# Optimization experiments

Measured on AMD Instinct MI355X. Metric: run time of the kernel, lower is better.

## Reference

```python
import jax, jax.numpy as jnp
import numpy as np

IN_FEATURES = 8192
OUT_FEATURES = 8192
CODESZ = 8
CB_SIZE = 256


def fwht(x):
    """Orthonormal Walsh-Hadamard transform along last dim (power of 2).
    Equivalent to x @ H / sqrt(n) with Sylvester Hadamard H (symmetric),
    so it implements both matmul_hadU and matmul_hadUt for K=1."""
    b, n = x.shape
    h = 2
    while h <= n:
        x = x.reshape(b, n // h, h)
        half = h // 2
        a, c = x[..., :half], x[..., half:]
        x = jnp.concatenate([a + c, a - c], axis=-1)
        h *= 2
    return x.reshape(b, n) * jnp.asarray(1.0 / np.sqrt(n), x.dtype)


def setup_inputs() -> dict:
    key = jax.random.key(0)
    ks = jax.random.split(key, 8)
    inp = jax.random.normal(ks[0], (32, 4, IN_FEATURES), dtype=jnp.float16)
    Qidxs = jax.random.randint(ks[1], (OUT_FEATURES, IN_FEATURES // CODESZ), 0, CB_SIZE, dtype=jnp.int32)
    codebook_table = jax.random.normal(ks[2], (CB_SIZE, CODESZ), dtype=jnp.float32).astype(jnp.float16)
    # positive per-column rescale (scaleWH buffer)
    scaleWH = (0.5 + jax.random.uniform(ks[3], (IN_FEATURES,), dtype=jnp.float32)).astype(jnp.float16)
    # random sign vectors SU/SV (stored as int8 +-1 in torch; used as fp16 multipliers)
    SU = jnp.where(jax.random.uniform(ks[4], (IN_FEATURES,)) < 0.5, -1.0, 1.0).astype(jnp.float16)
    SV = jnp.where(jax.random.uniform(ks[5], (OUT_FEATURES,)) < 0.5, -1.0, 1.0).astype(jnp.float16)
    Wscale = jnp.asarray(0.02, dtype=jnp.float16)
    bias = (0.01 * jax.random.normal(ks[6], (OUT_FEATURES,), dtype=jnp.float32)).astype(jnp.float16)
    return {"input": inp, "Qidxs": Qidxs, "codebook_table": codebook_table,
            "scaleWH": scaleWH, "SU": SU, "SV": SV, "Wscale": Wscale, "bias": bias}


def reference(input, Qidxs, codebook_table, scaleWH, SU, SV, Wscale, bias):
    x = input.reshape(-1, IN_FEATURES).astype(jnp.float16)
    # rescale_WH + SU sign flip, fused elementwise
    x = (x / scaleWH) * SU
    # matmul_hadUt_cuda (in_features is a power of 2 -> pure orthonormal WHT)
    x = fwht(x)
    # codebook dequant + GEMM: W_hat[o, i] = codebook[Qidxs[o, i//8], i%8] * Wscale
    W_hat = codebook_table[Qidxs].reshape(OUT_FEATURES, IN_FEATURES) * Wscale  # [out, in] fp16
    out = x @ W_hat.T  # [tokens, out]
    # matmul_hadU_cuda on output side (power of 2, no truncation needed)
    out = fwht(out)
    out = out * SV + bias
    return out.reshape(input.shape[:-1] + (OUT_FEATURES,))
```

## Files before the change

kernel.cpp:

```cpp
#include <hip/hip_runtime.h>
#include <hip/hip_bf16.h>

#define IN_F 8192
#define OUT_F 8192
#define NROWS 128
#define CB 256
#define NSL 8
#define KSLICE (IN_F / NSL)
#define NTB 128
#define QC (IN_F / 8)

using bf8   = __attribute__((ext_vector_type(8))) short;
using f32x4 = __attribute__((ext_vector_type(4))) float;

typedef const __attribute__((address_space(1))) void* as1cv;
typedef __attribute__((address_space(3))) void* as3v;

__device__ inline float bf2f(unsigned int u) {
    union { unsigned int i; float f; } v; v.i = u << 16; return v.f;
}
__device__ inline unsigned short f2bf(float f) {
    __hip_bfloat16 h = __float2bfloat16(f);
    return *reinterpret_cast<unsigned short*>(&h);
}
__device__ inline void unpack8(uint4 v, float* f) {
    f[0] = bf2f(v.x & 0xffffu); f[1] = bf2f(v.x >> 16);
    f[2] = bf2f(v.y & 0xffffu); f[3] = bf2f(v.y >> 16);
    f[4] = bf2f(v.z & 0xffffu); f[5] = bf2f(v.z >> 16);
    f[6] = bf2f(v.w & 0xffffu); f[7] = bf2f(v.w >> 16);
}

#define FWHT_SCALE 0.011048543456039806f

#define FWHT16(v)                                                         \
    _Pragma("unroll")                                                     \
    for (int hb = 0; hb < 4; ++hb) {                                      \
        const int hh = 1 << hb;                                           \
        _Pragma("unroll")                                                 \
        for (int j = 0; j < 16; ++j)                                      \
            if (!(j & hh)) {                                              \
                float a_ = v[j], b_ = v[j | hh];                          \
                v[j] = a_ + b_; v[j | hh] = a_ - b_;                      \
            }                                                             \
    }

__device__ inline void fwht4096(float* v, float* lds, int t) {
    FWHT16(v)
#pragma unroll
    for (int e = 0; e < 16; ++e) lds[e * 260 + t] = v[e];
    __syncthreads();
    {
        const int base = (t & 15) * 260 + (t >> 4) * 16;
#pragma unroll
        for (int q = 0; q < 4; ++q) {
            float4 f = *reinterpret_cast<const float4*>(&lds[base + q * 4]);
            v[q * 4 + 0] = f.x; v[q * 4 + 1] = f.y;
            v[q * 4 + 2] = f.z; v[q * 4 + 3] = f.w;
        }
    }
    FWHT16(v)
    __syncthreads();
    {
        const int e = t & 15, ub = t >> 4;
#pragma unroll
        for (int i = 0; i < 16; ++i) lds[e * 260 + i * 16 + ub] = v[i];
    }
    __syncthreads();
    {
        const int e = t & 15, i = t >> 4;
#pragma unroll
        for (int ub = 0; ub < 16; ++ub) v[ub] = lds[e * 260 + i * 16 + ub];
    }
    FWHT16(v)
    __syncthreads();
    {
        const int e = t & 15, i = t >> 4;
#pragma unroll
        for (int ub = 0; ub < 16; ++ub) lds[ub * 260 + i * 16 + e] = v[ub];
    }
    __syncthreads();
    {
        const int base = (t >> 4) * 260 + (t & 15) * 16;
#pragma unroll
        for (int q = 0; q < 4; ++q) {
            float4 f = *reinterpret_cast<const float4*>(&lds[base + q * 4]);
            v[q * 4 + 0] = f.x; v[q * 4 + 1] = f.y;
            v[q * 4 + 2] = f.z; v[q * 4 + 3] = f.w;
        }
    }
}

__global__ __launch_bounds__(256) void k_pre4(const float* __restrict__ in,
                                              const float* __restrict__ scaleWH,
                                              const float* __restrict__ SU,
                                              unsigned short* __restrict__ xt) {
    __shared__ float lds[4160];
    const int r = blockIdx.x, h = blockIdx.y, t = threadIdx.x;
    float v[16];
    const float4* xp = reinterpret_cast<const float4*>(in + (size_t)r * IN_F);
    const float4* sp = reinterpret_cast<const float4*>(scaleWH);
    const float4* up = reinterpret_cast<const float4*>(SU);
#pragma unroll
    for (int q = 0; q < 4; ++q) {
        float4 xl = xp[t * 4 + q],        sl = sp[t * 4 + q],        ul = up[t * 4 + q];
        float4 xh = xp[1024 + t * 4 + q], sh = sp[1024 + t * 4 + q], uh = up[1024 + t * 4 + q];
        float lo0 = xl.x / sl.x * ul.x, hi0 = xh.x / sh.x * uh.x;
        float lo1 = xl.y / sl.y * ul.y, hi1 = xh.y / sh.y * uh.y;
        float lo2 = xl.z / sl.z * ul.z, hi2 = xh.z / sh.z * uh.z;
        float lo3 = xl.w / sl.w * ul.w, hi3 = xh.w / sh.w * uh.w;
        v[q * 4 + 0] = h ? lo0 - hi0 : lo0 + hi0;
        v[q * 4 + 1] = h ? lo1 - hi1 : lo1 + hi1;
        v[q * 4 + 2] = h ? lo2 - hi2 : lo2 + hi2;
        v[q * 4 + 3] = h ? lo3 - hi3 : lo3 + hi3;
    }
    fwht4096(v, lds, t);
    const int ub = t >> 4, i = t & 15;
    const int kblk = h * 128 + ub * 8 + (i >> 1);
    const size_t base = ((size_t)(r >> 4) * 256 + kblk) * 512 + (size_t)(r & 15) * 8;
#pragma unroll
    for (int half = 0; half < 2; ++half) {
        unsigned int w[4];
#pragma unroll
        for (int p = 0; p < 4; ++p) {
            unsigned int lo = f2bf(v[half * 8 + 2 * p]     * FWHT_SCALE);
            unsigned int hi = f2bf(v[half * 8 + 2 * p + 1] * FWHT_SCALE);
            w[p] = lo | (hi << 16);
        }
        const int oct = (i & 1) * 2 + half;
        *reinterpret_cast<uint4*>(xt + base + oct * 128) = make_uint4(w[0], w[1], w[2], w[3]);
    }
}

__global__ __launch_bounds__(512, 4) void k_gemm9(
        const unsigned short* __restrict__ xt,
        const int* __restrict__ Qidxs,
        const float* __restrict__ cb,
        const float* __restrict__ wscale,
        unsigned short* __restrict__ pout) {
    __shared__ __align__(16) unsigned short cbl[CB][8];
    __shared__ __align__(16) int Qlds[2][128 * 64];
    const int tid = threadIdx.x;
    const int wave = tid >> 6, lane = tid & 63;
    const int wr = wave & 3, wc = wave >> 2;
    const int lr = lane & 15, lk8 = lane >> 4;
    const int n0 = blockIdx.x * NTB;
    const int ks0 = blockIdx.y * KSLICE;
    const int ksb = ks0 >> 5;
    const int c0 = ks0 >> 3;

    auto stageQ = [&](int buf, int ch) {
#pragma unroll
        for (int j = 0; j < 4; ++j) {
            const int row = j * 32 + wave * 4 + (lane >> 4);
            const int cgs = (lane & 15) ^ (row & 15);
            const int* g = Qidxs + (size_t)(n0 + row) * QC + c0 + ch * 64 + cgs * 4;
            as3v l = (as3v)(&Qlds[buf][(j * 32 + wave * 4) * 64]);
            __builtin_amdgcn_global_load_lds((as1cv)(const void*)g, l, 16, 0, 0);
        }
    };

    stageQ(0, 0);
    const float wsc = wscale[0];
    for (int e = tid; e < CB * 8; e += 512) cbl[e >> 3][e & 7] = f2bf(cb[e] * wsc);

    f32x4 acc[2][4];
#pragma unroll
    for (int mt = 0; mt < 2; ++mt)
#pragma unroll
        for (int nt = 0; nt < 4; ++nt) acc[mt][nt] = (f32x4){0.f, 0.f, 0.f, 0.f};

    const unsigned short* xw = xt + ((size_t)(wr * 2) * 256 + ksb) * 512 + lane * 8;
    __syncthreads();
    stageQ(1, 1);

#define CHUNK(BUF, CH)                                                        \
    _Pragma("unroll")                                                         \
    for (int itc = 0; itc < 16; ++itc) {                                      \
        const int it = (CH) * 16 + itc;                                       \
        const int qcol = ((itc ^ lr) << 2) + lk8;                             \
        const int qv0 = Qlds[BUF][(wc * 64 +  0 + lr) * 64 + qcol];           \
        const int qv1 = Qlds[BUF][(wc * 64 + 16 + lr) * 64 + qcol];           \
        const int qv2 = Qlds[BUF][(wc * 64 + 32 + lr) * 64 + qcol];           \
        const int qv3 = Qlds[BUF][(wc * 64 + 48 + lr) * 64 + qcol];           \
        bf8 a0 = *reinterpret_cast<const bf8*>(xw + ((size_t)(0 * 256) + it) * 512); \
        bf8 a1 = *reinterpret_cast<const bf8*>(xw + ((size_t)(1 * 256) + it) * 512); \
        bf8 b0 = *(const bf8*)&cbl[qv0][0];                                   \
        bf8 b1 = *(const bf8*)&cbl[qv1][0];                                   \
        bf8 b2 = *(const bf8*)&cbl[qv2][0];                                   \
        bf8 b3 = *(const bf8*)&cbl[qv3][0];                                   \
        acc[0][0] = __builtin_amdgcn_mfma_f32_16x16x32_bf16(a0, b0, acc[0][0], 0, 0, 0); \
        acc[0][1] = __builtin_amdgcn_mfma_f32_16x16x32_bf16(a0, b1, acc[0][1], 0, 0, 0); \
        acc[0][2] = __builtin_amdgcn_mfma_f32_16x16x32_bf16(a0, b2, acc[0][2], 0, 0, 0); \
        acc[0][3] = __builtin_amdgcn_mfma_f32_16x16x32_bf16(a0, b3, acc[0][3], 0, 0, 0); \
        acc[1][0] = __builtin_amdgcn_mfma_f32_16x16x32_bf16(a1, b0, acc[1][0], 0, 0, 0); \
        acc[1][1] = __builtin_amdgcn_mfma_f32_16x16x32_bf16(a1, b1, acc[1][1], 0, 0, 0); \
        acc[1][2] = __builtin_amdgcn_mfma_f32_16x16x32_bf16(a1, b2, acc[1][2], 0, 0, 0); \
        acc[1][3] = __builtin_amdgcn_mfma_f32_16x16x32_bf16(a1, b3, acc[1][3], 0, 0, 0); \
    }

    CHUNK(0, 0)
    __syncthreads();
    CHUNK(1, 1)
#undef CHUNK

    unsigned short* ps = pout + (size_t)blockIdx.y * (NROWS * OUT_F);
#pragma unroll
    for (int mt = 0; mt < 2; ++mt) {
        const int row = wr * 32 + mt * 16 + lk8 * 4;
#pragma unroll
        for (int nt = 0; nt < 4; ++nt) {
            const int col = n0 + wc * 64 + nt * 16 + lr;
#pragma unroll
            for (int r2 = 0; r2 < 4; ++r2)
                ps[(size_t)(row + r2) * OUT_F + col] = f2bf(acc[mt][nt][r2]);
        }
    }
}

__global__ __launch_bounds__(256) void k_post4(const unsigned short* __restrict__ pin,
                                               const float* __restrict__ SV,
                                               const float* __restrict__ bias,
                                               float* __restrict__ out) {
    __shared__ float lds[4160];
    const int r = blockIdx.x, h = blockIdx.y, t = threadIdx.x;
    float lo[16], hi[16], v[16];
#pragma unroll
    for (int j = 0; j < 16; ++j) { lo[j] = 0.f; hi[j] = 0.f; }
#pragma unroll 1
    for (int sl = 0; sl < NSL; ++sl) {
        const uint4* pl = reinterpret_cast<const uint4*>(
            pin + (size_t)sl * NROWS * OUT_F + (size_t)r * OUT_F + t * 16);
        const uint4* ph = reinterpret_cast<const uint4*>(
            pin + (size_t)sl * NROWS * OUT_F + (size_t)r * OUT_F + 4096 + t * 16);
        float a[8], b[8];
        unpack8(pl[0], a); unpack8(pl[1], b);
#pragma unroll
        for (int j = 0; j < 8; ++j) { lo[j] += a[j]; lo[8 + j] += b[j]; }
        unpack8(ph[0], a); unpack8(ph[1], b);
#pragma unroll
        for (int j = 0; j < 8; ++j) { hi[j] += a[j]; hi[8 + j] += b[j]; }
    }
#pragma unroll
    for (int j = 0; j < 16; ++j) v[j] = h ? lo[j] - hi[j] : lo[j] + hi[j];
    fwht4096(v, lds, t);
    const int cb4 = (h * 4096 + (t >> 4) * 256 + (t & 15) * 16) >> 2;
    const float4* svp = reinterpret_cast<const float4*>(SV);
    const float4* bip = reinterpret_cast<const float4*>(bias);
    float4* op = reinterpret_cast<float4*>(out + (size_t)r * OUT_F);
#pragma unroll
    for (int q = 0; q < 4; ++q) {
        float4 sv = svp[cb4 + q], bi = bip[cb4 + q], o;
        o.x = v[q * 4 + 0] * FWHT_SCALE * sv.x + bi.x;
        o.y = v[q * 4 + 1] * FWHT_SCALE * sv.y + bi.y;
        o.z = v[q * 4 + 2] * FWHT_SCALE * sv.z + bi.z;
        o.w = v[q * 4 + 3] * FWHT_SCALE * sv.w + bi.w;
        op[cb4 + q] = o;
    }
}

extern "C" void kernel_launch(void* const* d_in, const int* in_sizes, int n_in,
                              void* d_out, int out_size, void* d_ws, size_t ws_size,
                              hipStream_t stream) {
    const float* in      = (const float*)d_in[0];
    const int*   Qidxs   = (const int*)d_in[1];
    const float* cb      = (const float*)d_in[2];
    const float* scaleWH = (const float*)d_in[3];
    const float* SU      = (const float*)d_in[4];
    const float* SV      = (const float*)d_in[5];
    const float* wscale  = (const float*)d_in[6];
    const float* bias    = (const float*)d_in[7];
    float* out = (float*)d_out;

    unsigned short* xt    = (unsigned short*)d_ws;
    unsigned short* parts = (unsigned short*)((char*)d_ws
                            + (size_t)NROWS * IN_F * 2);

    k_pre4<<<dim3(NROWS, 2), 256, 0, stream>>>(in, scaleWH, SU, xt);
    k_gemm9<<<dim3(OUT_F / NTB, NSL), 512, 0, stream>>>(xt, Qidxs, cb, wscale, parts);
    k_post4<<<dim3(NROWS, 2), 256, 0, stream>>>(parts, SV, bias, out);
}
```

Baseline: 46.33 us.

## Switch codebook GEMM to 32x32x16 MFMA with 4 waves and software pipelining

Moves the GEMM from 16x16x32 MFMA tiles with 8 waves to 32x32x16 MFMA tiles with 4 waves, each wave owning 32 output columns and all 128 rows. The preprocessing kernel writes the activation layout to match the new A-operand fragment order. The inner loop is restructured to double-buffer codebook lookups and activation loads across even and odd k-steps. The aim is fewer LDS codebook gathers per FLOP and better latency hiding, at the cost of more accumulator registers and lower occupancy per block.

```diff
diff --git a/kernel.cpp b/kernel.cpp
--- a/kernel.cpp
+++ b/kernel.cpp
@@ -10,8 +10,8 @@
 #define NTB 128
 #define QC (IN_F / 8)
 
-using bf8   = __attribute__((ext_vector_type(8))) short;
-using f32x4 = __attribute__((ext_vector_type(4))) float;
+using bf8    = __attribute__((ext_vector_type(8))) short;
+using f32x16 = __attribute__((ext_vector_type(16))) float;
 
 typedef const __attribute__((address_space(1))) void* as1cv;
 typedef __attribute__((address_space(3))) void* as3v;
@@ -90,7 +90,7 @@
     }
 }
 
-__global__ __launch_bounds__(256) void k_pre4(const float* __restrict__ in,
+__global__ __launch_bounds__(256) void k_pre5(const float* __restrict__ in,
                                               const float* __restrict__ scaleWH,
                                               const float* __restrict__ SU,
                                               unsigned short* __restrict__ xt) {
@@ -114,9 +114,8 @@
         v[q * 4 + 3] = h ? lo3 - hi3 : lo3 + hi3;
     }
     fwht4096(v, lds, t);
-    const int ub = t >> 4, i = t & 15;
-    const int kblk = h * 128 + ub * 8 + (i >> 1);
-    const size_t base = ((size_t)(r >> 4) * 256 + kblk) * 512 + (size_t)(r & 15) * 8;
+    const int k0 = h * 4096 + (t >> 4) * 256 + (t & 15) * 16;
+    const size_t base = ((size_t)(r >> 5) * 512 + (k0 >> 4)) * 512 + (size_t)(r & 31) * 8;
 #pragma unroll
     for (int half = 0; half < 2; ++half) {
         unsigned int w[4];
@@ -126,95 +125,107 @@
             unsigned int hi = f2bf(v[half * 8 + 2 * p + 1] * FWHT_SCALE);
             w[p] = lo | (hi << 16);
         }
-        const int oct = (i & 1) * 2 + half;
-        *reinterpret_cast<uint4*>(xt + base + oct * 128) = make_uint4(w[0], w[1], w[2], w[3]);
-    }
-}
-
-__global__ __launch_bounds__(512, 4) void k_gemm9(
+        *reinterpret_cast<uint4*>(xt + base + half * 256) = make_uint4(w[0], w[1], w[2], w[3]);
+    }
+}
+
+__global__ __launch_bounds__(256, 2) void k_gemm12(
         const unsigned short* __restrict__ xt,
         const int* __restrict__ Qidxs,
         const float* __restrict__ cb,
         const float* __restrict__ wscale,
         unsigned short* __restrict__ pout) {
     __shared__ __align__(16) unsigned short cbl[CB][8];
-    __shared__ __align__(16) int Qlds[2][128 * 64];
+    __shared__ __align__(16) int Qlds[2][8192];
     const int tid = threadIdx.x;
     const int wave = tid >> 6, lane = tid & 63;
-    const int wr = wave & 3, wc = wave >> 2;
-    const int lr = lane & 15, lk8 = lane >> 4;
+    const int ln31 = lane & 31, lh = lane >> 5;
     const int n0 = blockIdx.x * NTB;
     const int ks0 = blockIdx.y * KSLICE;
-    const int ksb = ks0 >> 5;
+    const int ksb2 = ks0 >> 4;
     const int c0 = ks0 >> 3;
 
-    auto stageQ = [&](int buf, int ch) {
-#pragma unroll
-        for (int j = 0; j < 4; ++j) {
-            const int row = j * 32 + wave * 4 + (lane >> 4);
-            const int cgs = (lane & 15) ^ (row & 15);
-            const int* g = Qidxs + (size_t)(n0 + row) * QC + c0 + ch * 64 + cgs * 4;
-            as3v l = (as3v)(&Qlds[buf][(j * 32 + wave * 4) * 64]);
+    auto stageQ = [&](int h) {
+#pragma unroll
+        for (int j = 0; j < 8; ++j) {
+            const int row = j * 16 + wave * 4 + (lane >> 4);
+            const int cgs = (lane & 15) ^ (row & 7);
+            const int* g = Qidxs + (size_t)(n0 + row) * QC + c0 + h * 64 + cgs * 4;
+            as3v l = (as3v)(&Qlds[h][(j * 16 + wave * 4) * 64]);
             __builtin_amdgcn_global_load_lds((as1cv)(const void*)g, l, 16, 0, 0);
         }
     };
 
-    stageQ(0, 0);
+    stageQ(0);
     const float wsc = wscale[0];
-    for (int e = tid; e < CB * 8; e += 512) cbl[e >> 3][e & 7] = f2bf(cb[e] * wsc);
-
-    f32x4 acc[2][4];
-#pragma unroll
-    for (int mt = 0; mt < 2; ++mt)
-#pragma unroll
-        for (int nt = 0; nt < 4; ++nt) acc[mt][nt] = (f32x4){0.f, 0.f, 0.f, 0.f};
-
-    const unsigned short* xw = xt + ((size_t)(wr * 2) * 256 + ksb) * 512 + lane * 8;
-    __syncthreads();
-    stageQ(1, 1);
-
-#define CHUNK(BUF, CH)                                                        \
-    _Pragma("unroll")                                                         \
-    for (int itc = 0; itc < 16; ++itc) {                                      \
-        const int it = (CH) * 16 + itc;                                       \
-        const int qcol = ((itc ^ lr) << 2) + lk8;                             \
-        const int qv0 = Qlds[BUF][(wc * 64 +  0 + lr) * 64 + qcol];           \
-        const int qv1 = Qlds[BUF][(wc * 64 + 16 + lr) * 64 + qcol];           \
-        const int qv2 = Qlds[BUF][(wc * 64 + 32 + lr) * 64 + qcol];           \
-        const int qv3 = Qlds[BUF][(wc * 64 + 48 + lr) * 64 + qcol];           \
-        bf8 a0 = *reinterpret_cast<const bf8*>(xw + ((size_t)(0 * 256) + it) * 512); \
-        bf8 a1 = *reinterpret_cast<const bf8*>(xw + ((size_t)(1 * 256) + it) * 512); \
-        bf8 b0 = *(const bf8*)&cbl[qv0][0];                                   \
-        bf8 b1 = *(const bf8*)&cbl[qv1][0];                                   \
-        bf8 b2 = *(const bf8*)&cbl[qv2][0];                                   \
-        bf8 b3 = *(const bf8*)&cbl[qv3][0];                                   \
-        acc[0][0] = __builtin_amdgcn_mfma_f32_16x16x32_bf16(a0, b0, acc[0][0], 0, 0, 0); \
-        acc[0][1] = __builtin_amdgcn_mfma_f32_16x16x32_bf16(a0, b1, acc[0][1], 0, 0, 0); \
-        acc[0][2] = __builtin_amdgcn_mfma_f32_16x16x32_bf16(a0, b2, acc[0][2], 0, 0, 0); \
-        acc[0][3] = __builtin_amdgcn_mfma_f32_16x16x32_bf16(a0, b3, acc[0][3], 0, 0, 0); \
-        acc[1][0] = __builtin_amdgcn_mfma_f32_16x16x32_bf16(a1, b0, acc[1][0], 0, 0, 0); \
-        acc[1][1] = __builtin_amdgcn_mfma_f32_16x16x32_bf16(a1, b1, acc[1][1], 0, 0, 0); \
-        acc[1][2] = __builtin_amdgcn_mfma_f32_16x16x32_bf16(a1, b2, acc[1][2], 0, 0, 0); \
-        acc[1][3] = __builtin_amdgcn_mfma_f32_16x16x32_bf16(a1, b3, acc[1][3], 0, 0, 0); \
-    }
-
-    CHUNK(0, 0)
-    __syncthreads();
-    CHUNK(1, 1)
+    for (int e = tid; e < CB * 8; e += 256) cbl[e >> 3][e & 7] = f2bf(cb[e] * wsc);
+
+    f32x16 acc[4];
+#pragma unroll
+    for (int mt = 0; mt < 4; ++mt)
+#pragma unroll
+        for (int r2 = 0; r2 < 16; ++r2) acc[mt][r2] = 0.f;
+
+    const unsigned short* xw0 = xt + ((size_t)(0 * 512) + ksb2) * 512 + lane * 8;
+    const unsigned short* xw1 = xt + ((size_t)(1 * 512) + ksb2) * 512 + lane * 8;
+    const unsigned short* xw2 = xt + ((size_t)(2 * 512) + ksb2) * 512 + lane * 8;
+    const unsigned short* xw3 = xt + ((size_t)(3 * 512) + ksb2) * 512 + lane * 8;
+
+    const int qrow = wave * 32 + ln31;
+    const int qs7 = qrow & 7;
+    const int qb = qrow * 64;
+
+#define QR(H, ITL) (Qlds[H][qb + (((((ITL) * 2 + lh) >> 2) ^ qs7) << 2) + (((ITL) * 2 + lh) & 3)])
+#define GA(Q) (*(const bf8*)&cbl[(Q)][0])
+#define LA(D, IT) {                                                           \
+        D##0 = *(const bf8*)(xw0 + (size_t)(IT) * 512);                       \
+        D##1 = *(const bf8*)(xw1 + (size_t)(IT) * 512);                       \
+        D##2 = *(const bf8*)(xw2 + (size_t)(IT) * 512);                       \
+        D##3 = *(const bf8*)(xw3 + (size_t)(IT) * 512); }
+#define MFMA4(A_, B_) {                                                       \
+        acc[0] = __builtin_amdgcn_mfma_f32_32x32x16_bf16(A_##0, B_, acc[0], 0, 0, 0); \
+        acc[1] = __builtin_amdgcn_mfma_f32_32x32x16_bf16(A_##1, B_, acc[1], 0, 0, 0); \
+        acc[2] = __builtin_amdgcn_mfma_f32_32x32x16_bf16(A_##2, B_, acc[2], 0, 0, 0); \
+        acc[3] = __builtin_amdgcn_mfma_f32_32x32x16_bf16(A_##3, B_, acc[3], 0, 0, 0); }
+
+#define CHUNK(H) {                                                            \
+        int qE = QR(H, 0), qO = QR(H, 1);                                     \
+        bf8 aE0, aE1, aE2, aE3, aO0, aO1, aO2, aO3;                           \
+        LA(aE, (H) * 32 + 0) LA(aO, (H) * 32 + 1)                             \
+        bf8 bE = GA(qE), bO;                                                  \
+        _Pragma("unroll")                                                     \
+        for (int i2 = 0; i2 < 16; ++i2) {                                     \
+            const int itl = i2 * 2;                                           \
+            if (i2 < 15) qE = QR(H, itl + 2);                                 \
+            bO = GA(qO);                                                      \
+            MFMA4(aE, bE)                                                     \
+            if (i2 < 15) LA(aE, (H) * 32 + itl + 2)                           \
+            if (i2 < 15) qO = QR(H, itl + 3);                                 \
+            if (i2 < 15) bE = GA(qE);                                         \
+            MFMA4(aO, bO)                                                     \
+            if (i2 < 15) LA(aO, (H) * 32 + itl + 3)                           \
+        } }
+
+    __syncthreads();
+    stageQ(1);
+    CHUNK(0)
+    __syncthreads();
+    CHUNK(1)
 #undef CHUNK
+#undef MFMA4
+#undef LA
+#undef GA
+#undef QR
 
     unsigned short* ps = pout + (size_t)blockIdx.y * (NROWS * OUT_F);
-#pragma unroll
-    for (int mt = 0; mt < 2; ++mt) {
-        const int row = wr * 32 + mt * 16 + lk8 * 4;
-#pragma unroll
-        for (int nt = 0; nt < 4; ++nt) {
-            const int col = n0 + wc * 64 + nt * 16 + lr;
-#pragma unroll
-            for (int r2 = 0; r2 < 4; ++r2)
-                ps[(size_t)(row + r2) * OUT_F + col] = f2bf(acc[mt][nt][r2]);
-        }
-    }
+    const int col = n0 + wave * 32 + ln31;
+#pragma unroll
+    for (int mt = 0; mt < 4; ++mt)
+#pragma unroll
+        for (int r2 = 0; r2 < 16; ++r2) {
+            const int row = mt * 32 + (r2 & 3) + 8 * (r2 >> 2) + 4 * lh;
+            ps[(size_t)row * OUT_F + col] = f2bf(acc[mt][r2]);
+        }
 }
 
 __global__ __launch_bounds__(256) void k_post4(const unsigned short* __restrict__ pin,
@@ -275,7 +286,7 @@
     unsigned short* parts = (unsigned short*)((char*)d_ws
                             + (size_t)NROWS * IN_F * 2);
 
-    k_pre4<<<dim3(NROWS, 2), 256, 0, stream>>>(in, scaleWH, SU, xt);
-    k_gemm9<<<dim3(OUT_F / NTB, NSL), 512, 0, stream>>>(xt, Qidxs, cb, wscale, parts);
+    k_pre5<<<dim3(NROWS, 2), 256, 0, stream>>>(in, scaleWH, SU, xt);
+    k_gemm12<<<dim3(OUT_F / NTB, NSL), 256, 0, stream>>>(xt, Qidxs, cb, wscale, parts);
     k_post4<<<dim3(NROWS, 2), 256, 0, stream>>>(parts, SV, bias, out);
 }
```

Result: slower. 54.55 us (+17.8%).

## Split K into 16 slices, pack Qidxs to bytes in LDS, larger per-wave tiles

Applied to the files above, without the earlier changes.

The GEMM kernel now uses 16 K-slices with 256 threads per block instead of 8 slices with 512. Each wave computes a 64x64 output tile (4x4 MFMA tiles), which raises A/B operand reuse per codebook lookup. Qidxs are loaded with plain vector loads and packed four to a 32-bit word in a small swizzled LDS buffer, replacing the double-buffered async global-to-LDS staging. The trade-off is twice as many bf16 partial-sum buffers for the post kernel to read and reduce, plus higher register pressure from 64 accumulators per lane.

```diff
diff --git a/kernel.cpp b/kernel.cpp
--- a/kernel.cpp
+++ b/kernel.cpp
@@ -5,16 +5,14 @@
 #define OUT_F 8192
 #define NROWS 128
 #define CB 256
-#define NSL 8
-#define KSLICE (IN_F / NSL)
+#define NSL2 16
+#define NSLT 16
+#define KSLICE2 (IN_F / NSL2)
 #define NTB 128
 #define QC (IN_F / 8)
 
 using bf8   = __attribute__((ext_vector_type(8))) short;
 using f32x4 = __attribute__((ext_vector_type(4))) float;
-
-typedef const __attribute__((address_space(1))) void* as1cv;
-typedef __attribute__((address_space(3))) void* as3v;
 
 __device__ inline float bf2f(unsigned int u) {
     union { unsigned int i; float f; } v; v.i = u << 16; return v.f;
@@ -131,85 +129,106 @@
     }
 }
 
-__global__ __launch_bounds__(512, 4) void k_gemm9(
+__global__ __launch_bounds__(256, 3) void k_gemm17(
         const unsigned short* __restrict__ xt,
         const int* __restrict__ Qidxs,
         const float* __restrict__ cb,
         const float* __restrict__ wscale,
         unsigned short* __restrict__ pout) {
     __shared__ __align__(16) unsigned short cbl[CB][8];
-    __shared__ __align__(16) int Qlds[2][128 * 64];
+    __shared__ __align__(16) unsigned int Qb[128 * 16];
     const int tid = threadIdx.x;
     const int wave = tid >> 6, lane = tid & 63;
-    const int wr = wave & 3, wc = wave >> 2;
+    const int ngrp = wave & 1, mgrp = wave >> 1;
     const int lr = lane & 15, lk8 = lane >> 4;
     const int n0 = blockIdx.x * NTB;
-    const int ks0 = blockIdx.y * KSLICE;
+    const int ks0 = blockIdx.y * KSLICE2;
     const int ksb = ks0 >> 5;
     const int c0 = ks0 >> 3;
 
-    auto stageQ = [&](int buf, int ch) {
-#pragma unroll
-        for (int j = 0; j < 4; ++j) {
-            const int row = j * 32 + wave * 4 + (lane >> 4);
-            const int cgs = (lane & 15) ^ (row & 15);
-            const int* g = Qidxs + (size_t)(n0 + row) * QC + c0 + ch * 64 + cgs * 4;
-            as3v l = (as3v)(&Qlds[buf][(j * 32 + wave * 4) * 64]);
-            __builtin_amdgcn_global_load_lds((as1cv)(const void*)g, l, 16, 0, 0);
-        }
-    };
-
-    stageQ(0, 0);
+    {
+        const int row = tid >> 1, h = tid & 1;
+        const int* g = Qidxs + (size_t)(n0 + row) * QC + c0 + h * 32;
+        int q[32];
+#pragma unroll
+        for (int j4 = 0; j4 < 8; ++j4) {
+            int4 vv = *reinterpret_cast<const int4*>(g + j4 * 4);
+            q[j4 * 4 + 0] = vv.x; q[j4 * 4 + 1] = vv.y;
+            q[j4 * 4 + 2] = vv.z; q[j4 * 4 + 3] = vv.w;
+        }
+#pragma unroll
+        for (int s = 0; s < 4; ++s)
+#pragma unroll
+            for (int a2 = 0; a2 < 2; ++a2) {
+                unsigned int D = (unsigned int)(q[(a2 * 4 + 0) * 4 + s] & 255)
+                               | ((unsigned int)(q[(a2 * 4 + 1) * 4 + s] & 255) << 8)
+                               | ((unsigned int)(q[(a2 * 4 + 2) * 4 + s] & 255) << 16)
+                               | ((unsigned int)(q[(a2 * 4 + 3) * 4 + s] & 255) << 24);
+                const int a = h * 2 + a2;
+                Qb[row * 16 + s * 4 + (a ^ (row & 3))] = D;
+            }
+    }
     const float wsc = wscale[0];
-    for (int e = tid; e < CB * 8; e += 512) cbl[e >> 3][e & 7] = f2bf(cb[e] * wsc);
-
-    f32x4 acc[2][4];
-#pragma unroll
-    for (int mt = 0; mt < 2; ++mt)
+    for (int e = tid; e < CB * 8; e += 256) cbl[e >> 3][e & 7] = f2bf(cb[e] * wsc);
+
+    f32x4 acc[4][4];
+#pragma unroll
+    for (int mt = 0; mt < 4; ++mt)
 #pragma unroll
         for (int nt = 0; nt < 4; ++nt) acc[mt][nt] = (f32x4){0.f, 0.f, 0.f, 0.f};
 
-    const unsigned short* xw = xt + ((size_t)(wr * 2) * 256 + ksb) * 512 + lane * 8;
-    __syncthreads();
-    stageQ(1, 1);
-
-#define CHUNK(BUF, CH)                                                        \
-    _Pragma("unroll")                                                         \
-    for (int itc = 0; itc < 16; ++itc) {                                      \
-        const int it = (CH) * 16 + itc;                                       \
-        const int qcol = ((itc ^ lr) << 2) + lk8;                             \
-        const int qv0 = Qlds[BUF][(wc * 64 +  0 + lr) * 64 + qcol];           \
-        const int qv1 = Qlds[BUF][(wc * 64 + 16 + lr) * 64 + qcol];           \
-        const int qv2 = Qlds[BUF][(wc * 64 + 32 + lr) * 64 + qcol];           \
-        const int qv3 = Qlds[BUF][(wc * 64 + 48 + lr) * 64 + qcol];           \
-        bf8 a0 = *reinterpret_cast<const bf8*>(xw + ((size_t)(0 * 256) + it) * 512); \
-        bf8 a1 = *reinterpret_cast<const bf8*>(xw + ((size_t)(1 * 256) + it) * 512); \
-        bf8 b0 = *(const bf8*)&cbl[qv0][0];                                   \
-        bf8 b1 = *(const bf8*)&cbl[qv1][0];                                   \
-        bf8 b2 = *(const bf8*)&cbl[qv2][0];                                   \
-        bf8 b3 = *(const bf8*)&cbl[qv3][0];                                   \
-        acc[0][0] = __builtin_amdgcn_mfma_f32_16x16x32_bf16(a0, b0, acc[0][0], 0, 0, 0); \
-        acc[0][1] = __builtin_amdgcn_mfma_f32_16x16x32_bf16(a0, b1, acc[0][1], 0, 0, 0); \
-        acc[0][2] = __builtin_amdgcn_mfma_f32_16x16x32_bf16(a0, b2, acc[0][2], 0, 0, 0); \
-        acc[0][3] = __builtin_amdgcn_mfma_f32_16x16x32_bf16(a0, b3, acc[0][3], 0, 0, 0); \
-        acc[1][0] = __builtin_amdgcn_mfma_f32_16x16x32_bf16(a1, b0, acc[1][0], 0, 0, 0); \
-        acc[1][1] = __builtin_amdgcn_mfma_f32_16x16x32_bf16(a1, b1, acc[1][1], 0, 0, 0); \
-        acc[1][2] = __builtin_amdgcn_mfma_f32_16x16x32_bf16(a1, b2, acc[1][2], 0, 0, 0); \
-        acc[1][3] = __builtin_amdgcn_mfma_f32_16x16x32_bf16(a1, b3, acc[1][3], 0, 0, 0); \
-    }
-
-    CHUNK(0, 0)
-    __syncthreads();
-    CHUNK(1, 1)
-#undef CHUNK
+    const unsigned short* xw0 = xt + ((size_t)((mgrp * 4 + 0) * 256) + ksb) * 512 + lane * 8;
+    const unsigned short* xw1 = xt + ((size_t)((mgrp * 4 + 1) * 256) + ksb) * 512 + lane * 8;
+    const unsigned short* xw2 = xt + ((size_t)((mgrp * 4 + 2) * 256) + ksb) * 512 + lane * 8;
+    const unsigned short* xw3 = xt + ((size_t)((mgrp * 4 + 3) * 256) + ksb) * 512 + lane * 8;
+
+    __syncthreads();
+
+    unsigned int qr[4][4];
+#pragma unroll
+    for (int nb = 0; nb < 4; ++nb) {
+        const int qrow = ngrp * 64 + nb * 16 + lr;
+#pragma unroll
+        for (int a = 0; a < 4; ++a)
+            qr[nb][a] = Qb[qrow * 16 + lk8 * 4 + (a ^ (qrow & 3))];
+    }
+
+#pragma unroll
+    for (int i = 0; i < 16; ++i) {
+        const int sh = (i & 3) * 8;
+        bf8 b0 = *(const bf8*)&cbl[(qr[0][i >> 2] >> sh) & 255][0];
+        bf8 b1 = *(const bf8*)&cbl[(qr[1][i >> 2] >> sh) & 255][0];
+        bf8 b2 = *(const bf8*)&cbl[(qr[2][i >> 2] >> sh) & 255][0];
+        bf8 b3 = *(const bf8*)&cbl[(qr[3][i >> 2] >> sh) & 255][0];
+        bf8 a0 = *(const bf8*)(xw0 + (size_t)i * 512);
+        bf8 a1 = *(const bf8*)(xw1 + (size_t)i * 512);
+        bf8 a2 = *(const bf8*)(xw2 + (size_t)i * 512);
+        bf8 a3 = *(const bf8*)(xw3 + (size_t)i * 512);
+        acc[0][0] = __builtin_amdgcn_mfma_f32_16x16x32_bf16(a0, b0, acc[0][0], 0, 0, 0);
+        acc[0][1] = __builtin_amdgcn_mfma_f32_16x16x32_bf16(a0, b1, acc[0][1], 0, 0, 0);
+        acc[0][2] = __builtin_amdgcn_mfma_f32_16x16x32_bf16(a0, b2, acc[0][2], 0, 0, 0);
+        acc[0][3] = __builtin_amdgcn_mfma_f32_16x16x32_bf16(a0, b3, acc[0][3], 0, 0, 0);
+        acc[1][0] = __builtin_amdgcn_mfma_f32_16x16x32_bf16(a1, b0, acc[1][0], 0, 0, 0);
+        acc[1][1] = __builtin_amdgcn_mfma_f32_16x16x32_bf16(a1, b1, acc[1][1], 0, 0, 0);
+        acc[1][2] = __builtin_amdgcn_mfma_f32_16x16x32_bf16(a1, b2, acc[1][2], 0, 0, 0);
+        acc[1][3] = __builtin_amdgcn_mfma_f32_16x16x32_bf16(a1, b3, acc[1][3], 0, 0, 0);
+        acc[2][0] = __builtin_amdgcn_mfma_f32_16x16x32_bf16(a2, b0, acc[2][0], 0, 0, 0);
+        acc[2][1] = __builtin_amdgcn_mfma_f32_16x16x32_bf16(a2, b1, acc[2][1], 0, 0, 0);
+        acc[2][2] = __builtin_amdgcn_mfma_f32_16x16x32_bf16(a2, b2, acc[2][2], 0, 0, 0);
+        acc[2][3] = __builtin_amdgcn_mfma_f32_16x16x32_bf16(a2, b3, acc[2][3], 0, 0, 0);
+        acc[3][0] = __builtin_amdgcn_mfma_f32_16x16x32_bf16(a3, b0, acc[3][0], 0, 0, 0);
+        acc[3][1] = __builtin_amdgcn_mfma_f32_16x16x32_bf16(a3, b1, acc[3][1], 0, 0, 0);
+        acc[3][2] = __builtin_amdgcn_mfma_f32_16x16x32_bf16(a3, b2, acc[3][2], 0, 0, 0);
+        acc[3][3] = __builtin_amdgcn_mfma_f32_16x16x32_bf16(a3, b3, acc[3][3], 0, 0, 0);
+    }
 
     unsigned short* ps = pout + (size_t)blockIdx.y * (NROWS * OUT_F);
 #pragma unroll
-    for (int mt = 0; mt < 2; ++mt) {
-        const int row = wr * 32 + mt * 16 + lk8 * 4;
+    for (int mt = 0; mt < 4; ++mt) {
+        const int row = mgrp * 64 + mt * 16 + lk8 * 4;
 #pragma unroll
         for (int nt = 0; nt < 4; ++nt) {
-            const int col = n0 + wc * 64 + nt * 16 + lr;
+            const int col = n0 + ngrp * 64 + nt * 16 + lr;
 #pragma unroll
             for (int r2 = 0; r2 < 4; ++r2)
                 ps[(size_t)(row + r2) * OUT_F + col] = f2bf(acc[mt][nt][r2]);
@@ -217,7 +236,7 @@
     }
 }
 
-__global__ __launch_bounds__(256) void k_post4(const unsigned short* __restrict__ pin,
+__global__ __launch_bounds__(256) void k_post5(const unsigned short* __restrict__ pin,
                                                const float* __restrict__ SV,
                                                const float* __restrict__ bias,
                                                float* __restrict__ out) {
@@ -227,7 +246,7 @@
 #pragma unroll
     for (int j = 0; j < 16; ++j) { lo[j] = 0.f; hi[j] = 0.f; }
 #pragma unroll 1
-    for (int sl = 0; sl < NSL; ++sl) {
+    for (int sl = 0; sl < NSLT; ++sl) {
         const uint4* pl = reinterpret_cast<const uint4*>(
             pin + (size_t)sl * NROWS * OUT_F + (size_t)r * OUT_F + t * 16);
         const uint4* ph = reinterpret_cast<const uint4*>(
@@ -276,6 +295,6 @@
                             + (size_t)NROWS * IN_F * 2);
 
     k_pre4<<<dim3(NROWS, 2), 256, 0, stream>>>(in, scaleWH, SU, xt);
-    k_gemm9<<<dim3(OUT_F / NTB, NSL), 512, 0, stream>>>(xt, Qidxs, cb, wscale, parts);
-    k_post4<<<dim3(NROWS, 2), 256, 0, stream>>>(parts, SV, bias, out);
-}
+    k_gemm17<<<dim3(OUT_F / NTB, NSL2), 256, 0, stream>>>(xt, Qidxs, cb, wscale, parts);
+    k_post5<<<dim3(NROWS, 2), 256, 0, stream>>>(parts, SV, bias, out);
+}
```

Result: slower. 67.30 us (+45.3%).
